# Kernel optimization log

Measured on AMD Instinct MI355X. Metric: run time of the kernel, lower is better.

The kernel has to match this reference:

```python
import jax, jax.numpy as jnp
import numpy as np

D = 128
N_ATOMS = 200000
E_ATOMS = 800000
G = 2000            # num molecule graphs = nDrug + nProtein
N_BIG = 7000        # nDrug + nProtein + nSe
E_BIG = 200000
N_EMB = 100001


def _edges(key, n, e):
    # random edges guaranteed to have no self-loops (PyG convs strip/re-add them)
    k1, k2 = jax.random.split(key)
    src = jax.random.randint(k1, (e,), 0, n)
    off = jax.random.randint(k2, (e,), 1, n)
    return jnp.stack([src, (src + off) % n])


def setup_inputs() -> dict:
    key = jax.random.key(0)
    ks = jax.random.split(key, 40)
    s = 0.09  # ~1/sqrt(D) init scale
    nrm = lambda i, shape: jax.random.normal(ks[i], shape, dtype=jnp.float32) * s
    inp = {}
    inp['x_ids'] = jax.random.randint(ks[0], (N_BIG,), 0, N_EMB)
    inp['drugEdges'] = _edges(ks[1], N_BIG, E_BIG)
    inp['seEdges'] = _edges(ks[2], 5000, 1000)  # unused by forward
    inp['drugNodes'] = jax.random.randint(ks[3], (1000,), 0, N_BIG)
    inp['seNodes'] = jax.random.randint(ks[4], (5000,), 0, N_BIG)
    inp['proteinNodes'] = jax.random.randint(ks[5], (1000,), 0, N_EMB)
    inp['proteinWeight'] = jax.random.normal(ks[6], (1000,), dtype=jnp.float32)
    inp['atom_x'] = jax.random.randint(ks[7], (N_ATOMS,), 0, N_EMB)
    inp['atom_edge_index'] = _edges(ks[8], N_ATOMS, E_ATOMS)
    inp['atom_batch'] = jnp.sort(jax.random.randint(ks[9], (N_ATOMS,), 0, G))
    inp['nDrug'] = 1000
    inp['emb'] = jax.random.uniform(ks[10], (N_EMB, D), minval=0.001, maxval=0.3, dtype=jnp.float32)
    for i in range(3):
        inp[f'gatW{i+1}'] = nrm(11 + i, (D, D))
        inp[f'attS{i+1}'] = nrm(14 + i, (D,))
        inp[f'attD{i+1}'] = nrm(17 + i, (D,))
        inp[f'gatB{i+1}'] = nrm(20 + i, (D,))
        inp[f'poolP{i+1}'] = nrm(23 + i, (D,))
    inp['lin1_W'] = nrm(26, (2 * D, D))
    inp['lin1_b'] = nrm(27, (D,))
    inp['gcn1_W'] = nrm(28, (D, D))
    inp['gcn1_b'] = nrm(29, (D,))
    inp['gcn2_W'] = nrm(30, (D, D))
    inp['gcn2_b'] = nrm(31, (D,))
    return inp


def _gat(x, src, dst, n, W, a_s, a_d, b):
    # PyG GATConv, 1 head: h = xW; e_ij = LeakyReLU(a_s.h_j + a_d.h_i);
    # softmax over incoming edges of i (self-loops re-added); out_i = sum_j alpha_ij h_j + b
    h = x @ W
    loops = jnp.arange(n)
    s = jnp.concatenate([src, loops])
    d = jnp.concatenate([dst, loops])
    e = jax.nn.leaky_relu((h @ a_s)[s] + (h @ a_d)[d], 0.2)
    m = jax.ops.segment_max(e, d, num_segments=n)
    ex = jnp.exp(e - m[d])
    z = jax.ops.segment_sum(ex, d, num_segments=n)
    w = ex / z[d]
    return jax.ops.segment_sum(w[:, None] * h[s], d, num_segments=n) + b


def _gcn(x, src, dst, n, W, b):
    loops = jnp.arange(n)
    s = jnp.concatenate([src, loops])
    d = jnp.concatenate([dst, loops])
    deg = jax.ops.segment_sum(jnp.ones(d.shape[0], x.dtype), d, num_segments=n)
    dis = deg ** -0.5
    coef = dis[s] * dis[d]
    return jax.ops.segment_sum(coef[:, None] * (x @ W)[s], d, num_segments=n) + b


def _topk1(x, p):
    # TopKPooling with ratio=1: keep all nodes, gate by tanh of projection score
    score = (x @ p) / jnp.linalg.norm(p)
    return x * jnp.tanh(score)[:, None]


def _gmp_gap(x, batch, g):
    mx = jax.ops.segment_max(x, batch, num_segments=g)
    sm = jax.ops.segment_sum(x, batch, num_segments=g)
    cnt = jax.ops.segment_sum(jnp.ones((x.shape[0], 1), x.dtype), batch, num_segments=g)
    return jnp.concatenate([mx, sm / jnp.maximum(cnt, 1.0)], axis=1)


def reference(x_ids, drugEdges, seEdges, drugNodes, seNodes, proteinNodes, proteinWeight,
              atom_x, atom_edge_index, atom_batch, nDrug, emb,
              gatW1, attS1, attD1, gatB1, poolP1,
              gatW2, attS2, attD2, gatB2, poolP2,
              gatW3, attS3, attD3, gatB3, poolP3,
              lin1_W, lin1_b, gcn1_W, gcn1_b, gcn2_W, gcn2_b):
    na = atom_x.shape[0]
    asrc, adst = atom_edge_index[0], atom_edge_index[1]
    xa = emb[atom_x]                                   # [na, D]
    xa = jax.nn.relu(_gat(xa, asrc, adst, na, gatW1, attS1, attD1, gatB1))
    xa = _topk1(xa, poolP1)
    x1 = _gmp_gap(xa, atom_batch, G)                   # [G, 2D]
    xa = jax.nn.relu(_gat(xa, asrc, adst, na, gatW2, attS2, attD2, gatB2))
    xa = _topk1(xa, poolP2)
    x2 = _gmp_gap(xa, atom_batch, G)
    xa = jax.nn.relu(_gat(xa, asrc, adst, na, gatW3, attS3, attD3, gatB3))
    xa = _topk1(xa, poolP3)
    x3 = _gmp_gap(xa, atom_batch, G)
    xDP = jax.nn.relu((x1 + x2 + x3) @ lin1_W + lin1_b)  # [G, D]
    nProtein = proteinNodes.shape[0]
    xse = emb[x_ids[nDrug + nProtein:]]                # side-effect node embeddings
    xb = jnp.concatenate([xDP, xse], axis=0)           # [N_BIG, D]
    dsrc, ddst = drugEdges[0], drugEdges[1]
    xb = jax.nn.relu(_gcn(xb, dsrc, ddst, N_BIG, gcn1_W, gcn1_b))
    xb = jax.nn.relu(_gcn(xb, dsrc, ddst, N_BIG, gcn2_W, gcn2_b))
    return (xb[drugNodes], xb[seNodes], xb)
```

## Files before the change

### kernel.cpp

```cpp
#include <hip/hip_runtime.h>
#include <cfloat>
#include <cmath>

#define D 128
#define N_ATOMS 200000
#define E_ATOMS 800000
#define G_GROUPS 2000
#define N_BIG 7000
#define E_BIG 200000
#define N_ALL (N_ATOMS + N_BIG)
#define E_ALL (E_ATOMS + E_BIG)

static inline int ceil_div(int a, int b) { return (a + b - 1) / b; }

typedef __attribute__((ext_vector_type(8))) _Float16 f16x8;
typedef __attribute__((ext_vector_type(2))) _Float16 h2_t;
typedef __attribute__((ext_vector_type(4))) float f32x4;

__device__ inline h2_t u2h(unsigned u) { return __builtin_bit_cast(h2_t, u); }
__device__ inline unsigned h2u(h2_t h) { return __builtin_bit_cast(unsigned, h); }
__device__ inline unsigned packh2(float x, float y) {
  h2_t h;
  h[0] = (_Float16)x;
  h[1] = (_Float16)y;
  return h2u(h);
}
__device__ inline float leaky(float e) { return fmaxf(e, 0.2f * e); }
__device__ inline float fast_tanh(float x) {
  float cx = fminf(fmaxf(x, -15.f), 15.f);
  float t = __expf(2.f * cx);
  return (t - 1.f) * __frcp_rn(t + 1.f);
}

__global__ void count_all(const int* __restrict__ adst, const int* __restrict__ ddst, int* __restrict__ deg,
                          int* __restrict__ rank) {
  int i = blockIdx.x * 256 + threadIdx.x;
  if (i < E_ATOMS)
    rank[i] = atomicAdd(&deg[adst[i]], 1);
  else if (i < E_ALL)
    rank[i] = atomicAdd(&deg[N_ATOMS + ddst[i - E_ATOMS]], 1);
}

__global__ void fill_csx(const int* __restrict__ asrc, const int* __restrict__ adst,
                         const int* __restrict__ dsrc, const int* __restrict__ ddst,
                         const int* __restrict__ rpx, const int* __restrict__ rank, int* __restrict__ csx) {
  int i = blockIdx.x * 256 + threadIdx.x;
  if (i < E_ATOMS) {
    csx[rpx[adst[i]] + rank[i]] = asrc[i];
  } else if (i < E_ALL) {
    int k = i - E_ATOMS;
    csx[rpx[N_ATOMS + ddst[k]] + rank[i]] = dsrc[k];
  }
}

__global__ void fill_pad(const int* __restrict__ deg, const int* __restrict__ rpx, int* __restrict__ csx) {
  int d = blockIdx.x * 256 + threadIdx.x;
  if (d >= N_ALL) return;
  int dg = deg[d];
  int b = rpx[d], e = rpx[d + 1];
  int sv = (d < N_ATOMS) ? d : d - N_ATOMS;
  for (int j = b + dg; j < e; ++j) csx[j] = sv;
}

__global__ void make_cntp(const int* __restrict__ deg, int* __restrict__ cntp, int n) {
  int i = blockIdx.x * 256 + threadIdx.x;
  if (i < n) cntp[i] = (deg[i] + 8) & ~7;
}

__global__ __launch_bounds__(256) void scan_phase1(const int* __restrict__ in, int* __restrict__ out,
                                                   int* __restrict__ bsums, int n) {
  __shared__ int lds[256];
  int t = threadIdx.x;
  int base = blockIdx.x * 1024;
  int v[4];
  int s = 0;
#pragma unroll
  for (int j = 0; j < 4; ++j) {
    int i = base + t * 4 + j;
    v[j] = (i < n) ? in[i] : 0;
    s += v[j];
  }
  lds[t] = s;
  __syncthreads();
  for (int off = 1; off < 256; off <<= 1) {
    int x = (t >= off) ? lds[t - off] : 0;
    __syncthreads();
    lds[t] += x;
    __syncthreads();
  }
  int excl = lds[t] - s;
  if (t == 255) bsums[blockIdx.x] = lds[255];
  int run = excl;
#pragma unroll
  for (int j = 0; j < 4; ++j) {
    int i = base + t * 4 + j;
    if (i < n) out[i] = run;
    run += v[j];
  }
}

__global__ __launch_bounds__(256) void scan_phase2(int* __restrict__ bsums, int* __restrict__ total_out, int nb) {
  __shared__ int lds[256];
  int t = threadIdx.x;
  int s = (t < nb) ? bsums[t] : 0;
  lds[t] = s;
  __syncthreads();
  for (int off = 1; off < 256; off <<= 1) {
    int x = (t >= off) ? lds[t - off] : 0;
    __syncthreads();
    lds[t] += x;
    __syncthreads();
  }
  if (t < nb) bsums[t] = lds[t] - s;
  if (t == 255) total_out[0] = lds[255];
}

__global__ void scan_phase3(int* __restrict__ out, const int* __restrict__ bsums, int n) {
  int i = blockIdx.x * 256 + threadIdx.x;
  if (i < n) out[i] += bsums[i >> 10];
}

__global__ __launch_bounds__(256) void prep_kernel(const float* __restrict__ W0, const float* __restrict__ W1,
                                                   const float* __restrict__ W2, const float* __restrict__ W3,
                                                   const float* __restrict__ W4, unsigned short* __restrict__ Wsplit,
                                                   const float* __restrict__ p0, const float* __restrict__ p1,
                                                   const float* __restrict__ p2, float* __restrict__ pn) {
  int b = blockIdx.x;
  if (b < 5) {
    const float* W = (b == 0) ? W0 : (b == 1) ? W1 : (b == 2) ? W2 : (b == 3) ? W3 : W4;
    unsigned short* dstH = Wsplit + (size_t)b * 16384;
    int t = threadIdx.x;
    int col = t & 127;
    int half = t >> 7;
#pragma unroll
    for (int kg = 0; kg < 8; ++kg) {
      int k0 = kg * 16 + half * 8;
      f16x8 vh;
#pragma unroll
      for (int j = 0; j < 8; ++j) vh[j] = (_Float16)W[(k0 + j) * 128 + col];
      int byte_off = (col * 256 + k0 * 2) ^ ((col & 7) << 4);
      *(f16x8*)((char*)dstH + byte_off) = vh;
    }
  } else {
    int t = threadIdx.x;
    int g = t >> 6, lane = t & 63;
    if (g < 3) {
      const float* p = (g == 0) ? p0 : (g == 1) ? p1 : p2;
      float2 v = ((const float2*)p)[lane];
      float s = v.x * v.x + v.y * v.y;
#pragma unroll
      for (int off = 32; off; off >>= 1) s += __shfl_xor(s, off);
      if (lane == 0) pn[g] = 1.f / sqrtf(s);
    }
  }
}

__global__ __launch_bounds__(512) void gemm_f16(const unsigned short* __restrict__ A,
                                                const unsigned short* __restrict__ Wsp,
                                                unsigned short* __restrict__ H, float* __restrict__ hs,
                                                float* __restrict__ hd, const float* __restrict__ aS,
                                                const float* __restrict__ aD, int M) {
  __shared__ unsigned short Wl[16384];
  int t = threadIdx.x;
  {
    const uint4* src = (const uint4*)Wsp;
    uint4* dst = (uint4*)Wl;
#pragma unroll
    for (int i = 0; i < 4; ++i) dst[t + i * 512] = src[t + i * 512];
  }
  __syncthreads();
  int wave = t >> 6, lane = t & 63;
  int lr = lane & 15, lq = lane >> 4;
  int row0 = blockIdx.x * 256 + wave * 32;
  f32x4 acc[2][8];
#pragma unroll
  for (int rt = 0; rt < 2; ++rt)
#pragma unroll
    for (int ct = 0; ct < 8; ++ct) acc[rt][ct] = (f32x4){0.f, 0.f, 0.f, 0.f};

#pragma unroll
  for (int ks = 0; ks < 4; ++ks) {
    int k8 = ks * 32 + lq * 8;
    f16x8 Af[2];
#pragma unroll
    for (int rt = 0; rt < 2; ++rt) {
      int row = row0 + rt * 16 + lr;
      if (row < M) {
        Af[rt] = *(const f16x8*)(A + (size_t)row * D + k8);
      } else {
        Af[rt] = (f16x8){0, 0, 0, 0, 0, 0, 0, 0};
      }
    }
#pragma unroll
    for (int ct = 0; ct < 8; ++ct) {
      int col = ct * 16 + lr;
      int byte_off = (col * 256 + k8 * 2) ^ ((col & 7) << 4);
      f16x8 Bh = *(f16x8*)((char*)Wl + byte_off);
#pragma unroll
      for (int rt = 0; rt < 2; ++rt)
        acc[rt][ct] = __builtin_amdgcn_mfma_f32_16x16x32_f16(Af[rt], Bh, acc[rt][ct], 0, 0, 0);
    }
  }
#pragma unroll
  for (int rt = 0; rt < 2; ++rt)
#pragma unroll
    for (int ct = 0; ct < 8; ++ct) {
      int col = ct * 16 + lr;
#pragma unroll
      for (int i = 0; i < 4; ++i) {
        int row = row0 + rt * 16 + lq * 4 + i;
        if (row < M) {
          _Float16 hv = (_Float16)acc[rt][ct][i];
          H[(size_t)row * D + col] = __builtin_bit_cast(unsigned short, hv);
        }
      }
    }
  if (aS) {
    float sA[8], sD[8];
#pragma unroll
    for (int ct = 0; ct < 8; ++ct) {
      sA[ct] = aS[ct * 16 + lr];
      sD[ct] = aD[ct * 16 + lr];
    }
#pragma unroll
    for (int rt = 0; rt < 2; ++rt)
#pragma unroll
      for (int i = 0; i < 4; ++i) {
        float ps = 0.f, pd = 0.f;
#pragma unroll
        for (int ct = 0; ct < 8; ++ct) {
          ps = fmaf(acc[rt][ct][i], sA[ct], ps);
          pd = fmaf(acc[rt][ct][i], sD[ct], pd);
        }
#pragma unroll
        for (int off = 1; off < 16; off <<= 1) {
          ps += __shfl_xor(ps, off);
          pd += __shfl_xor(pd, off);
        }
        int row = row0 + rt * 16 + lq * 4 + i;
        if (lr == 0 && row < M) {
          hs[row] = ps;
          hd[row] = pd;
        }
      }
  }
}

__global__ void edge_weights(const float* __restrict__ hs, const float* __restrict__ hd,
                             const int* __restrict__ rpx, const int* __restrict__ deg,
                             const int* __restrict__ csx, unsigned* __restrict__ wts,
                             float* __restrict__ invz, int N) {
  int d = blockIdx.x * 256 + threadIdx.x;
  if (d >= N) return;
  int b = rpx[d];
  int cnt = rpx[d + 1] - b;
  int dg = deg[d];
  float hdd = hd[d];
  float es = leaky(hs[d] + hdd);
  float m = es;
  float* wf = (float*)wts;
  for (int j = 0; j < dg; ++j) {
    float e = leaky(hs[csx[b + j]] + hdd);
    wf[b + j] = e;
    m = fmaxf(m, e);
  }
  float z = 0.f;
  for (int j = 0; j < dg; ++j) {
    float w = __expf(wf[b + j] - m);
    z += w;
    wts[b + j] = packh2(w, w);
  }
  float wself = __expf(es - m);
  wts[b + dg] = packh2(wself, wself);
  z += wself;
  for (int j = dg + 1; j < cnt; ++j) wts[b + j] = 0;
  invz[d] = 1.f / z;
}

__global__ void gcn_weights(const int* __restrict__ rpx, const int* __restrict__ deg,
                            const int* __restrict__ csx, const float* __restrict__ dis,
                            unsigned* __restrict__ wtsG, int N) {
  int dl = blockIdx.x * 256 + threadIdx.x;
  if (dl >= N) return;
  int d = N_ATOMS + dl;
  int b = rpx[d];
  int cnt = rpx[d + 1] - b;
  int dg = deg[d];
  float dd = dis[dl];
  for (int j = 0; j < dg; ++j) {
    float w = dis[csx[b + j]] * dd;
    wtsG[b + j] = packh2(w, w);
  }
  wtsG[b + dg] = packh2(dd * dd, dd * dd);
  for (int j = dg + 1; j < cnt; ++j) wtsG[b + j] = 0;
}

__global__ __launch_bounds__(256) void gat_gather(const unsigned short* __restrict__ H,
                                                  const int* __restrict__ rpx, const int* __restrict__ csx,
                                                  const unsigned* __restrict__ wts,
                                                  const float* __restrict__ invz, const float* __restrict__ bias,
                                                  const float* __restrict__ poolP, const float* __restrict__ pnL,
                                                  unsigned short* __restrict__ Xout, int N) {
  int wid = (blockIdx.x * 256 + threadIdx.x) >> 6;
  int d = __builtin_amdgcn_readfirstlane(wid);
  if (d >= N) return;
  int lane = threadIdx.x & 63;
  int rb = rpx[d];
  int cnt = rpx[d + 1] - rb;
  const unsigned* H2 = (const unsigned*)H;
  float ax = 0.f, ay = 0.f;
  for (int i = 0; i < cnt; i += 8) {
    int s0 = csx[rb + i + 0], s1 = csx[rb + i + 1], s2 = csx[rb + i + 2], s3 = csx[rb + i + 3];
    int s4 = csx[rb + i + 4], s5 = csx[rb + i + 5], s6 = csx[rb + i + 6], s7 = csx[rb + i + 7];
    unsigned w0 = wts[rb + i + 0], w1 = wts[rb + i + 1], w2 = wts[rb + i + 2], w3 = wts[rb + i + 3];
    unsigned w4 = wts[rb + i + 4], w5 = wts[rb + i + 5], w6 = wts[rb + i + 6], w7 = wts[rb + i + 7];
    unsigned h0 = H2[(size_t)s0 * 64 + lane];
    unsigned h1 = H2[(size_t)s1 * 64 + lane];
    unsigned h2 = H2[(size_t)s2 * 64 + lane];
    unsigned h3 = H2[(size_t)s3 * 64 + lane];
    unsigned h4 = H2[(size_t)s4 * 64 + lane];
    unsigned h5 = H2[(size_t)s5 * 64 + lane];
    unsigned h6 = H2[(size_t)s6 * 64 + lane];
    unsigned h7 = H2[(size_t)s7 * 64 + lane];
    h2_t a2 = u2h(w0) * u2h(h0);
    a2 = __builtin_fmaf16(u2h(w1)[0], u2h(h1)[0], a2[0]) == a2[0] ? a2 : a2;
    a2 += u2h(w1) * u2h(h1);
    a2 += u2h(w2) * u2h(h2);
    a2 += u2h(w3) * u2h(h3);
    h2_t b2h = u2h(w4) * u2h(h4);
    b2h += u2h(w5) * u2h(h5);
    b2h += u2h(w6) * u2h(h6);
    b2h += u2h(w7) * u2h(h7);
    a2 += b2h;
    ax += (float)a2[0];
    ay += (float)a2[1];
  }
  float iz = invz[d];
  float2 b2 = ((const float2*)bias)[lane];
  ax = fmaxf(fmaf(ax, iz, b2.x), 0.f);
  ay = fmaxf(fmaf(ay, iz, b2.y), 0.f);
  float2 p2 = ((const float2*)poolP)[lane];
  float dot = ax * p2.x + ay * p2.y;
#pragma unroll
  for (int off = 32; off; off >>= 1) dot += __shfl_xor(dot, off);
  float sc = fast_tanh(dot * pnL[0]);
  ((unsigned*)Xout)[(size_t)d * 64 + lane] = packh2(ax * sc, ay * sc);
}

__global__ __launch_bounds__(256) void gcn_gather(const unsigned short* __restrict__ Y,
                                                  const int* __restrict__ rpx, const int* __restrict__ csx,
                                                  const unsigned* __restrict__ wtsG, const float* __restrict__ b,
                                                  unsigned short* __restrict__ outB, float* __restrict__ outF,
                                                  int N) {
  int wid = (blockIdx.x * 256 + threadIdx.x) >> 6;
  int dl = __builtin_amdgcn_readfirstlane(wid);
  if (dl >= N) return;
  int lane = threadIdx.x & 63;
  int rb = rpx[N_ATOMS + dl];
  int cnt = rpx[N_ATOMS + dl + 1] - rb;
  const unsigned* Y2 = (const unsigned*)Y;
  float ax = 0.f, ay = 0.f;
  for (int i = 0; i < cnt; i += 8) {
    int s0 = csx[rb + i + 0], s1 = csx[rb + i + 1], s2 = csx[rb + i + 2], s3 = csx[rb + i + 3];
    int s4 = csx[rb + i + 4], s5 = csx[rb + i + 5], s6 = csx[rb + i + 6], s7 = csx[rb + i + 7];
    unsigned w0 = wtsG[rb + i + 0], w1 = wtsG[rb + i + 1], w2 = wtsG[rb + i + 2], w3 = wtsG[rb + i + 3];
    unsigned w4 = wtsG[rb + i + 4], w5 = wtsG[rb + i + 5], w6 = wtsG[rb + i + 6], w7 = wtsG[rb + i + 7];
    unsigned h0 = Y2[(size_t)s0 * 64 + lane];
    unsigned h1 = Y2[(size_t)s1 * 64 + lane];
    unsigned h2 = Y2[(size_t)s2 * 64 + lane];
    unsigned h3 = Y2[(size_t)s3 * 64 + lane];
    unsigned h4 = Y2[(size_t)s4 * 64 + lane];
    unsigned h5 = Y2[(size_t)s5 * 64 + lane];
    unsigned h6 = Y2[(size_t)s6 * 64 + lane];
    unsigned h7 = Y2[(size_t)s7 * 64 + lane];
    h2_t a2 = u2h(w0) * u2h(h0);
    a2 += u2h(w1) * u2h(h1);
    a2 += u2h(w2) * u2h(h2);
    a2 += u2h(w3) * u2h(h3);
    h2_t b2h = u2h(w4) * u2h(h4);
    b2h += u2h(w5) * u2h(h5);
    b2h += u2h(w6) * u2h(h6);
    b2h += u2h(w7) * u2h(h7);
    a2 += b2h;
    ax += (float)a2[0];
    ay += (float)a2[1];
  }
  float2 b2 = ((const float2*)b)[lane];
  float ox = fmaxf(ax + b2.x, 0.f);
  float oy = fmaxf(ay + b2.y, 0.f);
  if (outF)
    ((float2*)outF)[(size_t)dl * 64 + lane] = make_float2(ox, oy);
  else
    ((unsigned*)outB)[(size_t)dl * 64 + lane] = packh2(ox, oy);
}

__global__ void group_bounds(const int* __restrict__ batch, int* __restrict__ gs, int* __restrict__ ge, int n) {
  int i = blockIdx.x * 256 + threadIdx.x;
  if (i >= n) return;
  int b = batch[i];
  if (i == 0 || batch[i - 1] != b) gs[b] = i;
  if (i == n - 1 || batch[i + 1] != b) ge[b] = i + 1;
}

__global__ __launch_bounds__(256) void pool_kernel(const unsigned short* __restrict__ X,
                                                   const int* __restrict__ gs, const int* __restrict__ ge,
                                                   float* __restrict__ x123) {
  __shared__ float2 mxs[4][64];
  __shared__ float2 sms[4][64];
  int g = blockIdx.x;
  int wv = threadIdx.x >> 6;
  int p = threadIdx.x & 63;
  int beg = gs[g], end = ge[g];
  int cnt = end - beg;
  const unsigned* X2 = (const unsigned*)X;
  float mx0 = -FLT_MAX, mx1 = -FLT_MAX, sm0 = 0.f, sm1 = 0.f;
  for (int i = beg + wv; i < end; i += 4) {
    h2_t v = u2h(X2[(size_t)i * 64 + p]);
    float a = (float)v[0], b = (float)v[1];
    mx0 = fmaxf(mx0, a);
    mx1 = fmaxf(mx1, b);
    sm0 += a;
    sm1 += b;
  }
  mxs[wv][p] = make_float2(mx0, mx1);
  sms[wv][p] = make_float2(sm0, sm1);
  __syncthreads();
  if (threadIdx.x < 64 && cnt > 0) {
#pragma unroll
    for (int k = 1; k < 4; ++k) {
      float2 m2 = mxs[k][p], s2 = sms[k][p];
      mx0 = fmaxf(mx0, m2.x);
      mx1 = fmaxf(mx1, m2.y);
      sm0 += s2.x;
      sm1 += s2.y;
    }
    float inv = 1.f / (float)cnt;
    float* xg = x123 + (size_t)g * 256;
    xg[2 * p] += mx0;
    xg[2 * p + 1] += mx1;
    xg[128 + 2 * p] += sm0 * inv;
    xg[128 + 2 * p + 1] += sm1 * inv;
  }
}

__global__ __launch_bounds__(128) void lin1_kernel(const float* __restrict__ x123, const float* __restrict__ W,
                                                   const float* __restrict__ b, unsigned short* __restrict__ xb) {
  __shared__ float row[256];
  int g = blockIdx.x;
  int c = threadIdx.x;
  row[c] = x123[(size_t)g * 256 + c];
  row[c + 128] = x123[(size_t)g * 256 + 128 + c];
  __syncthreads();
  float acc = b[c];
#pragma unroll 8
  for (int k = 0; k < 256; ++k) acc = fmaf(row[k], W[k * 128 + c], acc);
  _Float16 hv = (_Float16)fmaxf(acc, 0.f);
  xb[(size_t)g * D + c] = __builtin_bit_cast(unsigned short, hv);
}

__global__ void xse_kernel(const float* __restrict__ emb, const int* __restrict__ x_ids,
                           const int* __restrict__ nDrugPtr, int nProtein, unsigned short* __restrict__ xb) {
  int idx = blockIdx.x * 256 + threadIdx.x;
  int r = idx >> 6, lane = idx & 63;
  int off = nDrugPtr[0] + nProtein;
  int id = x_ids[off + r];
  float2 v = ((const float2*)(emb + (size_t)id * D))[lane];
  ((unsigned*)xb)[(size_t)(G_GROUPS + r) * 64 + lane] = packh2(v.x, v.y);
}

__global__ void dis_kernel(const int* __restrict__ deg, float* __restrict__ dis, int n) {
  int i = blockIdx.x * 256 + threadIdx.x;
  if (i < n) dis[i] = 1.f / sqrtf((float)(deg[N_ATOMS + i] + 1));
}

__global__ void gather_emb(const float* __restrict__ emb, const int* __restrict__ ids,
                           unsigned short* __restrict__ out, int n) {
  int idx = blockIdx.x * 256 + threadIdx.x;
  int node = idx >> 5, lane = idx & 31;
  if (node >= n) return;
  float4 v = ((const float4*)(emb + (size_t)ids[node] * D))[lane];
  uint2 o;
  o.x = packh2(v.x, v.y);
  o.y = packh2(v.z, v.w);
  ((uint2*)out)[(size_t)node * 32 + lane] = o;
}

__global__ void out_gather(const float* __restrict__ xb, const int* __restrict__ dn, const int* __restrict__ sn,
                           float* __restrict__ out) {
  int idx = blockIdx.x * 256 + threadIdx.x;
  int r = idx >> 6, lane = idx & 63;
  int s = (r < 1000) ? dn[r] : (r < 6000) ? sn[r - 1000] : (r - 6000);
  ((float2*)out)[(size_t)idx] = ((const float2*)(xb + (size_t)s * D))[lane];
}

extern "C" void kernel_launch(void* const* d_in, const int* in_sizes, int n_in, void* d_out, int out_size,
                              void* d_ws, size_t ws_size, hipStream_t stream) {
  const int* x_ids = (const int*)d_in[0];
  const int* drugE = (const int*)d_in[1];
  const int* drugNodes = (const int*)d_in[3];
  const int* seNodes = (const int*)d_in[4];
  int nProtein = in_sizes[5];
  const int* atom_x = (const int*)d_in[7];
  const int* atomE = (const int*)d_in[8];
  const int* atom_batch = (const int*)d_in[9];
  const int* nDrugPtr = (const int*)d_in[10];
  const float* emb = (const float*)d_in[11];
  const float* gatW[3] = {(const float*)d_in[12], (const float*)d_in[17], (const float*)d_in[22]};
  const float* attS[3] = {(const float*)d_in[13], (const float*)d_in[18], (const float*)d_in[23]};
  const float* attD[3] = {(const float*)d_in[14], (const float*)d_in[19], (const float*)d_in[24]};
  const float* gatB[3] = {(const float*)d_in[15], (const float*)d_in[20], (const float*)d_in[25]};
  const float* poolP[3] = {(const float*)d_in[16], (const float*)d_in[21], (const float*)d_in[26]};
  const float* lin1_W = (const float*)d_in[27];
  const float* lin1_b = (const float*)d_in[28];
  const float* gcn1_W = (const float*)d_in[29];
  const float* gcn1_b = (const float*)d_in[30];
  const float* gcn2_W = (const float*)d_in[31];
  const float* gcn2_b = (const float*)d_in[32];
  float* out = (float*)d_out;
  (void)n_in; (void)out_size; (void)ws_size;

  const int MAXX = E_ALL + 8 * N_ALL;

  char* ws = (char*)d_ws;
  size_t off = 0;
  auto alloc = [&](size_t bytes) -> char* {
    char* p = ws + off;
    off += (bytes + 255) & ~(size_t)255;
    return p;
  };
  unsigned short* bufA = (unsigned short*)alloc((size_t)N_ATOMS * D * 2);
  unsigned short* bufB = (unsigned short*)alloc((size_t)N_ATOMS * D * 2);
  float* hs = (float*)alloc((size_t)N_ATOMS * 4);
  float* hd = (float*)alloc((size_t)N_ATOMS * 4);
  int* csx = (int*)alloc((size_t)MAXX * 4);
  unsigned* wts = (unsigned*)alloc((size_t)MAXX * 4);
  unsigned* wtsG = (unsigned*)alloc((size_t)MAXX * 4);
  int* rank = (int*)alloc((size_t)E_ALL * 4);
  float* invz = (float*)alloc((size_t)N_ATOMS * 4);
  float* x123 = (float*)alloc((size_t)G_GROUPS * 256 * 4);
  unsigned short* xb1 = (unsigned short*)alloc((size_t)N_BIG * D * 2);
  unsigned short* xb2 = (unsigned short*)alloc((size_t)N_BIG * D * 2);
  float* xbF = (float*)alloc((size_t)N_BIG * D * 4);
  unsigned short* Wsplit = (unsigned short*)alloc((size_t)5 * 16384 * 2);
  int* rpx = (int*)alloc((size_t)(N_ALL + 1) * 4);
  int* deg = (int*)alloc((size_t)N_ALL * 4);
  int* cntp = (int*)alloc((size_t)N_ALL * 4);
  float* disB = (float*)alloc((size_t)N_BIG * 4);
  int* gs = (int*)alloc((size_t)G_GROUPS * 4);
  int* ge = (int*)alloc((size_t)G_GROUPS * 4);
  int* bsums = (int*)alloc(256 * 4);
  float* pn = (float*)alloc(256);

  const int* asrc = atomE;
  const int* adst = atomE + E_ATOMS;
  const int* dsrc = drugE;
  const int* ddst = drugE + E_BIG;

  prep_kernel<<<6, 256, 0, stream>>>(gatW[0], gatW[1], gatW[2], gcn1_W, gcn2_W, Wsplit, poolP[0], poolP[1],
                                     poolP[2], pn);

  hipMemsetAsync(deg, 0, (size_t)N_ALL * 4, stream);
  count_all<<<ceil_div(E_ALL, 256), 256, 0, stream>>>(adst, ddst, deg, rank);
  make_cntp<<<ceil_div(N_ALL, 256), 256, 0, stream>>>(deg, cntp, N_ALL);
  scan_phase1<<<ceil_div(N_ALL, 1024), 256, 0, stream>>>(cntp, rpx, bsums, N_ALL);
  scan_phase2<<<1, 256, 0, stream>>>(bsums, rpx + N_ALL, ceil_div(N_ALL, 1024));
  scan_phase3<<<ceil_div(N_ALL, 256), 256, 0, stream>>>(rpx, bsums, N_ALL);
  dis_kernel<<<ceil_div(N_BIG, 256), 256, 0, stream>>>(deg, disB, N_BIG);
  fill_csx<<<ceil_div(E_ALL, 256), 256, 0, stream>>>(asrc, adst, dsrc, ddst, rpx, rank, csx);
  fill_pad<<<ceil_div(N_ALL, 256), 256, 0, stream>>>(deg, rpx, csx);
  gcn_weights<<<ceil_div(N_BIG, 256), 256, 0, stream>>>(rpx, deg, csx, disB, wtsG, N_BIG);

  hipMemsetAsync(gs, 0, (size_t)G_GROUPS * 4, stream);
  hipMemsetAsync(ge, 0, (size_t)G_GROUPS * 4, stream);
  group_bounds<<<ceil_div(N_ATOMS, 256), 256, 0, stream>>>(atom_batch, gs, ge, N_ATOMS);

  gather_emb<<<ceil_div(N_ATOMS * 32, 256), 256, 0, stream>>>(emb, atom_x, bufA, N_ATOMS);
  hipMemsetAsync(x123, 0, (size_t)G_GROUPS * 256 * 4, stream);

  for (int L = 0; L < 3; ++L) {
    gemm_f16<<<ceil_div(N_ATOMS, 256), 512, 0, stream>>>(bufA, Wsplit + (size_t)L * 16384, bufB, hs, hd,
                                                         attS[L], attD[L], N_ATOMS);
    edge_weights<<<ceil_div(N_ATOMS, 256), 256, 0, stream>>>(hs, hd, rpx, deg, csx, wts, invz, N_ATOMS);
    gat_gather<<<N_ATOMS * 64 / 256, 256, 0, stream>>>(bufB, rpx, csx, wts, invz, gatB[L], poolP[L], pn + L,
                                                       bufA, N_ATOMS);
    pool_kernel<<<G_GROUPS, 256, 0, stream>>>(bufA, gs, ge, x123);
  }

  lin1_kernel<<<G_GROUPS, 128, 0, stream>>>(x123, lin1_W, lin1_b, xb1);
  xse_kernel<<<(N_BIG - G_GROUPS) * 64 / 256, 256, 0, stream>>>(emb, x_ids, nDrugPtr, nProtein, xb1);

  gemm_f16<<<ceil_div(N_BIG, 256), 512, 0, stream>>>(xb1, Wsplit + (size_t)3 * 16384, bufB, nullptr, nullptr,
                                                     nullptr, nullptr, N_BIG);
  gcn_gather<<<N_BIG * 64 / 256, 256, 0, stream>>>(bufB, rpx, csx, wtsG, gcn1_b, xb2, nullptr, N_BIG);
  gemm_f16<<<ceil_div(N_BIG, 256), 512, 0, stream>>>(xb2, Wsplit + (size_t)4 * 16384, bufB, nullptr, nullptr,
                                                     nullptr, nullptr, N_BIG);
  gcn_gather<<<N_BIG * 64 / 256, 256, 0, stream>>>(bufB, rpx, csx, wtsG, gcn2_b, nullptr, xbF, N_BIG);

  out_gather<<<13000 * 64 / 256, 256, 0, stream>>>(xbF, drugNodes, seNodes, out);
}
```

Before: 526.8 us.

## Fuse GAT edge softmax into gather kernel using wave-level reductions

Removes the separate per-node edge_weights kernel, which had one thread per node loop serially over its edges and write fp16 weights and inverse normalizers to global memory. Each wave in the gather kernel now computes the leaky scores, max and sum for its own node with lane-parallel shuffles, then broadcasts each weight to all lanes through __shfl. Nodes with more than 64 padded neighbours take a slower scalar path. The dis computation is also merged into the count post-processing kernel, removing one launch.

```diff
diff --git a/kernel.cpp b/kernel.cpp
--- a/kernel.cpp
+++ b/kernel.cpp
@@ -62,9 +62,10 @@
   for (int j = b + dg; j < e; ++j) csx[j] = sv;
 }
 
-__global__ void make_cntp(const int* __restrict__ deg, int* __restrict__ cntp, int n) {
+__global__ void post_count(const int* __restrict__ deg, int* __restrict__ cntp, float* __restrict__ dis) {
   int i = blockIdx.x * 256 + threadIdx.x;
-  if (i < n) cntp[i] = (deg[i] + 8) & ~7;
+  if (i < N_ALL) cntp[i] = (deg[i] + 8) & ~7;
+  if (i < N_BIG) dis[i] = 1.f / sqrtf((float)(deg[N_ATOMS + i] + 1));
 }
 
 __global__ __launch_bounds__(256) void scan_phase1(const int* __restrict__ in, int* __restrict__ out,
@@ -244,37 +245,6 @@
         }
       }
   }
-}
-
-__global__ void edge_weights(const float* __restrict__ hs, const float* __restrict__ hd,
-                             const int* __restrict__ rpx, const int* __restrict__ deg,
-                             const int* __restrict__ csx, unsigned* __restrict__ wts,
-                             float* __restrict__ invz, int N) {
-  int d = blockIdx.x * 256 + threadIdx.x;
-  if (d >= N) return;
-  int b = rpx[d];
-  int cnt = rpx[d + 1] - b;
-  int dg = deg[d];
-  float hdd = hd[d];
-  float es = leaky(hs[d] + hdd);
-  float m = es;
-  float* wf = (float*)wts;
-  for (int j = 0; j < dg; ++j) {
-    float e = leaky(hs[csx[b + j]] + hdd);
-    wf[b + j] = e;
-    m = fmaxf(m, e);
-  }
-  float z = 0.f;
-  for (int j = 0; j < dg; ++j) {
-    float w = __expf(wf[b + j] - m);
-    z += w;
-    wts[b + j] = packh2(w, w);
-  }
-  float wself = __expf(es - m);
-  wts[b + dg] = packh2(wself, wself);
-  z += wself;
-  for (int j = dg + 1; j < cnt; ++j) wts[b + j] = 0;
-  invz[d] = 1.f / z;
 }
 
 __global__ void gcn_weights(const int* __restrict__ rpx, const int* __restrict__ deg,
@@ -295,47 +265,85 @@
   for (int j = dg + 1; j < cnt; ++j) wtsG[b + j] = 0;
 }
 
-__global__ __launch_bounds__(256) void gat_gather(const unsigned short* __restrict__ H,
-                                                  const int* __restrict__ rpx, const int* __restrict__ csx,
-                                                  const unsigned* __restrict__ wts,
-                                                  const float* __restrict__ invz, const float* __restrict__ bias,
-                                                  const float* __restrict__ poolP, const float* __restrict__ pnL,
-                                                  unsigned short* __restrict__ Xout, int N) {
+__global__ __launch_bounds__(256) void gat_fused(const unsigned short* __restrict__ H,
+                                                 const int* __restrict__ rpx, const int* __restrict__ deg,
+                                                 const int* __restrict__ csx, const float* __restrict__ hs,
+                                                 const float* __restrict__ hd, const float* __restrict__ bias,
+                                                 const float* __restrict__ poolP, const float* __restrict__ pnL,
+                                                 unsigned short* __restrict__ Xout, int N) {
   int wid = (blockIdx.x * 256 + threadIdx.x) >> 6;
   int d = __builtin_amdgcn_readfirstlane(wid);
   if (d >= N) return;
   int lane = threadIdx.x & 63;
   int rb = rpx[d];
   int cnt = rpx[d + 1] - rb;
+  int dg = deg[d];
+  float hdd = hd[d];
   const unsigned* H2 = (const unsigned*)H;
   float ax = 0.f, ay = 0.f;
-  for (int i = 0; i < cnt; i += 8) {
-    int s0 = csx[rb + i + 0], s1 = csx[rb + i + 1], s2 = csx[rb + i + 2], s3 = csx[rb + i + 3];
-    int s4 = csx[rb + i + 4], s5 = csx[rb + i + 5], s6 = csx[rb + i + 6], s7 = csx[rb + i + 7];
-    unsigned w0 = wts[rb + i + 0], w1 = wts[rb + i + 1], w2 = wts[rb + i + 2], w3 = wts[rb + i + 3];
-    unsigned w4 = wts[rb + i + 4], w5 = wts[rb + i + 5], w6 = wts[rb + i + 6], w7 = wts[rb + i + 7];
-    unsigned h0 = H2[(size_t)s0 * 64 + lane];
-    unsigned h1 = H2[(size_t)s1 * 64 + lane];
-    unsigned h2 = H2[(size_t)s2 * 64 + lane];
-    unsigned h3 = H2[(size_t)s3 * 64 + lane];
-    unsigned h4 = H2[(size_t)s4 * 64 + lane];
-    unsigned h5 = H2[(size_t)s5 * 64 + lane];
-    unsigned h6 = H2[(size_t)s6 * 64 + lane];
-    unsigned h7 = H2[(size_t)s7 * 64 + lane];
-    h2_t a2 = u2h(w0) * u2h(h0);
-    a2 = __builtin_fmaf16(u2h(w1)[0], u2h(h1)[0], a2[0]) == a2[0] ? a2 : a2;
-    a2 += u2h(w1) * u2h(h1);
-    a2 += u2h(w2) * u2h(h2);
-    a2 += u2h(w3) * u2h(h3);
-    h2_t b2h = u2h(w4) * u2h(h4);
-    b2h += u2h(w5) * u2h(h5);
-    b2h += u2h(w6) * u2h(h6);
-    b2h += u2h(w7) * u2h(h7);
-    a2 += b2h;
-    ax += (float)a2[0];
-    ay += (float)a2[1];
-  }
-  float iz = invz[d];
+  float iz;
+  if (cnt <= 64) {
+    float e = -FLT_MAX;
+    if (lane < dg)
+      e = leaky(hs[csx[rb + lane]] + hdd);
+    else if (lane == dg)
+      e = leaky(hs[d] + hdd);
+    float m = e;
+#pragma unroll
+    for (int off = 32; off; off >>= 1) m = fmaxf(m, __shfl_xor(m, off));
+    float w = (lane <= dg) ? __expf(e - m) : 0.f;
+    float z = w;
+#pragma unroll
+    for (int off = 32; off; off >>= 1) z += __shfl_xor(z, off);
+    iz = 1.f / z;
+    unsigned wpk = packh2(w, w);
+    for (int i = 0; i < cnt; i += 8) {
+      int s0 = csx[rb + i + 0], s1 = csx[rb + i + 1], s2 = csx[rb + i + 2], s3 = csx[rb + i + 3];
+      int s4 = csx[rb + i + 4], s5 = csx[rb + i + 5], s6 = csx[rb + i + 6], s7 = csx[rb + i + 7];
+      unsigned w0 = __shfl(wpk, i + 0), w1 = __shfl(wpk, i + 1), w2 = __shfl(wpk, i + 2),
+               w3 = __shfl(wpk, i + 3), w4 = __shfl(wpk, i + 4), w5 = __shfl(wpk, i + 5),
+               w6 = __shfl(wpk, i + 6), w7 = __shfl(wpk, i + 7);
+      unsigned h0 = H2[(size_t)s0 * 64 + lane];
+      unsigned h1 = H2[(size_t)s1 * 64 + lane];
+      unsigned h2 = H2[(size_t)s2 * 64 + lane];
+      unsigned h3 = H2[(size_t)s3 * 64 + lane];
+      unsigned h4 = H2[(size_t)s4 * 64 + lane];
+      unsigned h5 = H2[(size_t)s5 * 64 + lane];
+      unsigned h6 = H2[(size_t)s6 * 64 + lane];
+      unsigned h7 = H2[(size_t)s7 * 64 + lane];
+      h2_t a2 = u2h(w0) * u2h(h0);
+      a2 += u2h(w1) * u2h(h1);
+      a2 += u2h(w2) * u2h(h2);
+      a2 += u2h(w3) * u2h(h3);
+      h2_t b2h = u2h(w4) * u2h(h4);
+      b2h += u2h(w5) * u2h(h5);
+      b2h += u2h(w6) * u2h(h6);
+      b2h += u2h(w7) * u2h(h7);
+      a2 += b2h;
+      ax += (float)a2[0];
+      ay += (float)a2[1];
+    }
+  } else {
+    float ml = -FLT_MAX;
+    for (int j = lane; j < dg; j += 64) ml = fmaxf(ml, leaky(hs[csx[rb + j]] + hdd));
+    if (lane == 0) ml = fmaxf(ml, leaky(hs[d] + hdd));
+#pragma unroll
+    for (int off = 32; off; off >>= 1) ml = fmaxf(ml, __shfl_xor(ml, off));
+    float zl = 0.f;
+    for (int j = lane; j < dg; j += 64) zl += __expf(leaky(hs[csx[rb + j]] + hdd) - ml);
+    if (lane == 0) zl += __expf(leaky(hs[d] + hdd) - ml);
+#pragma unroll
+    for (int off = 32; off; off >>= 1) zl += __shfl_xor(zl, off);
+    iz = 1.f / zl;
+    for (int i = 0; i <= dg; ++i) {
+      int s = csx[rb + i];
+      float ev = (i < dg) ? leaky(hs[s] + hdd) : leaky(hs[d] + hdd);
+      float wv = __expf(ev - ml);
+      h2_t hv = u2h(H2[(size_t)s * 64 + lane]);
+      ax = fmaf(wv, (float)hv[0], ax);
+      ay = fmaf(wv, (float)hv[1], ay);
+    }
+  }
   float2 b2 = ((const float2*)bias)[lane];
   ax = fmaxf(fmaf(ax, iz, b2.x), 0.f);
   ay = fmaxf(fmaf(ay, iz, b2.y), 0.f);
@@ -468,11 +476,6 @@
   ((unsigned*)xb)[(size_t)(G_GROUPS + r) * 64 + lane] = packh2(v.x, v.y);
 }
 
-__global__ void dis_kernel(const int* __restrict__ deg, float* __restrict__ dis, int n) {
-  int i = blockIdx.x * 256 + threadIdx.x;
-  if (i < n) dis[i] = 1.f / sqrtf((float)(deg[N_ATOMS + i] + 1));
-}
-
 __global__ void gather_emb(const float* __restrict__ emb, const int* __restrict__ ids,
                            unsigned short* __restrict__ out, int n) {
   int idx = blockIdx.x * 256 + threadIdx.x;
@@ -533,10 +536,8 @@
   float* hs = (float*)alloc((size_t)N_ATOMS * 4);
   float* hd = (float*)alloc((size_t)N_ATOMS * 4);
   int* csx = (int*)alloc((size_t)MAXX * 4);
-  unsigned* wts = (unsigned*)alloc((size_t)MAXX * 4);
   unsigned* wtsG = (unsigned*)alloc((size_t)MAXX * 4);
   int* rank = (int*)alloc((size_t)E_ALL * 4);
-  float* invz = (float*)alloc((size_t)N_ATOMS * 4);
   float* x123 = (float*)alloc((size_t)G_GROUPS * 256 * 4);
   unsigned short* xb1 = (unsigned short*)alloc((size_t)N_BIG * D * 2);
   unsigned short* xb2 = (unsigned short*)alloc((size_t)N_BIG * D * 2);
@@ -561,11 +562,10 @@
 
   hipMemsetAsync(deg, 0, (size_t)N_ALL * 4, stream);
   count_all<<<ceil_div(E_ALL, 256), 256, 0, stream>>>(adst, ddst, deg, rank);
-  make_cntp<<<ceil_div(N_ALL, 256), 256, 0, stream>>>(deg, cntp, N_ALL);
+  post_count<<<ceil_div(N_ALL, 256), 256, 0, stream>>>(deg, cntp, disB);
   scan_phase1<<<ceil_div(N_ALL, 1024), 256, 0, stream>>>(cntp, rpx, bsums, N_ALL);
   scan_phase2<<<1, 256, 0, stream>>>(bsums, rpx + N_ALL, ceil_div(N_ALL, 1024));
   scan_phase3<<<ceil_div(N_ALL, 256), 256, 0, stream>>>(rpx, bsums, N_ALL);
-  dis_kernel<<<ceil_div(N_BIG, 256), 256, 0, stream>>>(deg, disB, N_BIG);
   fill_csx<<<ceil_div(E_ALL, 256), 256, 0, stream>>>(asrc, adst, dsrc, ddst, rpx, rank, csx);
   fill_pad<<<ceil_div(N_ALL, 256), 256, 0, stream>>>(deg, rpx, csx);
   gcn_weights<<<ceil_div(N_BIG, 256), 256, 0, stream>>>(rpx, deg, csx, disB, wtsG, N_BIG);
@@ -580,9 +580,8 @@
   for (int L = 0; L < 3; ++L) {
     gemm_f16<<<ceil_div(N_ATOMS, 256), 512, 0, stream>>>(bufA, Wsplit + (size_t)L * 16384, bufB, hs, hd,
                                                          attS[L], attD[L], N_ATOMS);
-    edge_weights<<<ceil_div(N_ATOMS, 256), 256, 0, stream>>>(hs, hd, rpx, deg, csx, wts, invz, N_ATOMS);
-    gat_gather<<<N_ATOMS * 64 / 256, 256, 0, stream>>>(bufB, rpx, csx, wts, invz, gatB[L], poolP[L], pn + L,
-                                                       bufA, N_ATOMS);
+    gat_fused<<<N_ATOMS * 64 / 256, 256, 0, stream>>>(bufB, rpx, deg, csx, hs, hd, gatB[L], poolP[L], pn + L,
+                                                      bufA, N_ATOMS);
     pool_kernel<<<G_GROUPS, 256, 0, stream>>>(bufA, gs, ge, x123);
   }
 
```

Result: slower. 541.6 us (+2.8%).
